# Optimization experiments

Hardware: AMD Instinct MI355X
Metric: run time of the kernel (lower is better)

## Reference

```python
import jax, jax.numpy as jnp
import numpy as np
import math

N_RAYS = 16384
HIDDEN = 32
Z_BOUNDS = (0.1, 1.0, 10.0)
STEPS_FIRST = (128, 64)
N_IMPORTANCE = 128
ALPHA_IMP = 0.02
INNER, OUTER = 1.0, 2.0


def _uniform_z_log():
    # get_uniform_z_vals: per-segment log10 linspace, endpoint excluded like torch code
    segs = []
    for i in range(len(STEPS_FIRST)):
        lo, hi = math.log10(Z_BOUNDS[i]), math.log10(Z_BOUNDS[i + 1])
        segs.append(np.linspace(lo, hi - (hi - lo) / STEPS_FIRST[i], STEPS_FIRST[i], dtype=np.float32))
    return jnp.asarray(np.concatenate(segs))


def _density(x, Wd1, bd1, Wd2, bd2):
    hfeat = jax.nn.relu(x @ Wd1 + bd1)            # [N,S,HIDDEN]
    sigma = jax.nn.softplus(hfeat @ Wd2 + bd2)[..., 0]  # [N,S]
    return sigma, hfeat


def _mip_scale(x):
    # mipnerf360_scale with translation_center = 0
    dist = jnp.linalg.norm(x, axis=-1, keepdims=True)
    scale = jnp.where(dist > INNER, (OUTER - (OUTER - INNER) / dist) / dist, 1.0)
    return x * scale


def _sample_points(rays_o, rays_d, z_vals):
    pts = rays_o[:, None, :] + rays_d[:, None, :] * z_vals[..., None]  # [N,S,3]
    dirs = rays_d / jnp.linalg.norm(rays_d, axis=-1, keepdims=True)
    return pts, jnp.broadcast_to(dirs[:, None, :], pts.shape)


def _weights_from_sigma(sigmas, z_log):
    # render_rays_log compositing: delta[:, -1] = 0
    delta = jnp.concatenate([z_log[:, 1:] - z_log[:, :-1], jnp.zeros_like(z_log[:, :1])], axis=-1)
    alpha = 1.0 - jnp.exp(-sigmas * delta)
    alpha_shift = jnp.concatenate([jnp.zeros_like(alpha[:, :1]), alpha[:, :-1]], axis=-1)
    weights = alpha * jnp.cumprod(1.0 - alpha_shift, axis=-1)
    return weights


def _reweight(weights):
    z = jnp.zeros_like(weights[:, :1])
    wp = jnp.concatenate([z, weights, z], axis=-1)
    w = 0.5 * (jnp.maximum(wp[:, :-2], wp[:, 1:-1]) + jnp.maximum(wp[:, 1:-1], wp[:, 2:]))
    w = w + ALPHA_IMP / w.shape[-1]
    total = sum(STEPS_FIRST)
    seg_scale = jnp.concatenate([jnp.full((s,), s / total, w.dtype) for s in STEPS_FIRST])
    w = w * seg_scale
    return w / jnp.sum(w, axis=-1, keepdims=True)


def _sample_pdf(z_vals, weights, key):
    n_rays = z_vals.shape[0]
    cdf = jnp.cumsum(weights, axis=-1)
    z_mid = 0.5 * (z_vals[:, :-1] + z_vals[:, 1:])
    u = jnp.linspace(0.0, 1.0 - 1.0 / N_IMPORTANCE, N_IMPORTANCE, dtype=z_vals.dtype)
    u = u[None, :] + jax.random.uniform(key, (n_rays, N_IMPORTANCE), dtype=z_vals.dtype) / N_IMPORTANCE
    u = u * (cdf[:, -2:-1] - cdf[:, 1:2]) + cdf[:, 1:2]
    inds = jax.vmap(lambda c, uu: jnp.searchsorted(c, uu, side='right'))(cdf[:, 1:-2], u) + 1
    g = lambda arr, idx: jnp.take_along_axis(arr, idx, axis=1)
    cdf_b, cdf_a = g(cdf, inds - 1), g(cdf, inds)
    t = (u - cdf_b) / (cdf_a - cdf_b)
    zb, za = g(z_mid, inds - 1), g(z_mid, inds)
    return zb + (za - zb) * t


def _forward(n, h, w, K, E, bg_color, Wd1, bd1, Wd2, bd2, Wc1, bc1, Wc2, bc2):
    # get_rays
    dirs = jnp.stack([w + 0.5, h + 0.5, jnp.ones_like(w)], axis=-1)        # [N,3]
    cam_dirs = dirs @ jnp.linalg.inv(K).T
    rays_d = jnp.einsum('nij,nj->ni', E[:, :3, :3], cam_dirs)
    rays_o = E[:, :3, -1]
    # efficient_sampling (no-grad coarse pass)
    n_rays = rays_o.shape[0]
    z_log_c = jnp.broadcast_to(_uniform_z_log()[None, :], (n_rays, sum(STEPS_FIRST)))
    z_c = jnp.power(10.0, z_log_c)
    xyz_c, _ = _sample_points(rays_o, rays_d, z_c)
    sig_c, _ = _density(_mip_scale(xyz_c), Wd1, bd1, Wd2, bd2)
    w_c = _weights_from_sigma(sig_c, z_log_c)
    w_re = _reweight(w_c)
    z_log_f = jax.lax.stop_gradient(_sample_pdf(z_log_c, w_re, jax.random.key(42)))
    z_f = jnp.power(10.0, z_log_f)
    # fine pass through model
    xyz, dirs_f = _sample_points(rays_o, rays_d, z_f)
    sigma, hfeat = _density(_mip_scale(xyz), Wd1, bd1, Wd2, bd2)
    feat = jnp.concatenate([hfeat, dirs_f], axis=-1)
    rgbs = jax.nn.sigmoid(jax.nn.relu(feat @ Wc1 + bc1) @ Wc2 + bc2)       # [N,S,3]
    weights = _weights_from_sigma(sigma, z_log_f)
    image = jnp.sum(weights[..., None] * rgbs, axis=-2)
    invdepth = jnp.sum(weights / z_f, axis=-1)
    image = image + (1.0 - jnp.sum(weights, axis=-1, keepdims=True)) * bg_color
    lo, hi = math.log10(Z_BOUNDS[0]), math.log10(Z_BOUNDS[-1])
    z_log_s = (z_log_f - lo) / (hi - lo)
    return image, weights, z_log_s, invdepth


def setup_inputs() -> dict:
    key = jax.random.key(0)
    ks = jax.random.split(key, 12)
    N = N_RAYS
    h = jax.random.uniform(ks[0], (N,), dtype=jnp.float32) * 1080.0
    w = jax.random.uniform(ks[1], (N,), dtype=jnp.float32) * 1920.0
    f = 1000.0
    K = jnp.array([[f, 0.0, 960.0], [0.0, f, 540.0], [0.0, 0.0, 1.0]], jnp.float32)
    t = jax.random.normal(ks[2], (N, 3), dtype=jnp.float32) * 0.1
    E = jnp.tile(jnp.eye(4, dtype=jnp.float32)[None], (N, 1, 1)).at[:, :3, 3].set(t)
    n = jax.random.randint(ks[3], (N,), 0, 100)
    bg_color = jax.random.uniform(ks[4], (3,), dtype=jnp.float32)
    Wd1 = jax.random.normal(ks[5], (3, HIDDEN), dtype=jnp.float32) * 0.5
    bd1 = jnp.zeros((HIDDEN,), jnp.float32)
    Wd2 = jax.random.normal(ks[6], (HIDDEN, 1), dtype=jnp.float32) * 0.3
    bd2 = jnp.zeros((1,), jnp.float32)
    Wc1 = jax.random.normal(ks[7], (HIDDEN + 3, HIDDEN), dtype=jnp.float32) * 0.3
    bc1 = jnp.zeros((HIDDEN,), jnp.float32)
    Wc2 = jax.random.normal(ks[8], (HIDDEN, 3), dtype=jnp.float32) * 0.3
    bc2 = jnp.zeros((3,), jnp.float32)
    return {"n": n, "h": h, "w": w, "K": K, "E": E, "bg_color": bg_color,
            "Wd1": Wd1, "bd1": bd1, "Wd2": Wd2, "bd2": bd2,
            "Wc1": Wc1, "bc1": bc1, "Wc2": Wc2, "bc2": bc2}


def reference(n, h, w, K, E, bg_color, Wd1, bd1, Wd2, bd2, Wc1, bc1, Wc2, bc2):
    return _forward(n, h, w, K, E, bg_color, Wd1, bd1, Wd2, bd2, Wc1, bc1, Wc2, bc2)
```

## Files before the change

kernel.cpp:

```cpp
#include <hip/hip_runtime.h>
#include <stdint.h>

#define SC 192
#define SF 128
#define NT 128

#define WD1   0
#define BD1   96
#define WD2   128
#define BD2   160
#define BC2   161
#define NV4   164
#define W24   292
#define KIV   420
#define WDF   432
#define SWTOT 448

#define WS_FRAG_OFF 2048
#define WS_NEED     4096

#define RGBS 4

using half8 = __attribute__((ext_vector_type(8))) _Float16;
using f32x4 = __attribute__((ext_vector_type(4))) float;
using f32x2 = __attribute__((ext_vector_type(2))) float;

__device__ __forceinline__ float zlog_c(int t) {
  return (t < 128) ? (-1.0f + (float)t * 0.0078125f)
                   : ((float)(t - 128) * 0.015625f);
}
__device__ __forceinline__ float delta_c(int t) {
  if (t >= SC - 1) return 0.0f;
  return zlog_c(t + 1) - zlog_c(t);
}

__device__ __forceinline__ float fast_rcp(float x) { return __builtin_amdgcn_rcpf(x); }
__device__ __forceinline__ float fast_rsq(float x) { return __builtin_amdgcn_rsqf(x); }
__device__ __forceinline__ float exp10_f(float x) { return __expf(x * 2.30258509299f); }
__device__ __forceinline__ float softplus_f(float x) {
  return fmaxf(x, 0.0f) + __logf(1.0f + __expf(-fabsf(x)));
}

__device__ __forceinline__ f32x2 pk_fma2(f32x2 a, f32x2 b, f32x2 c) {
  f32x2 d;
  asm("v_pk_fma_f32 %0, %1, %2, %3" : "=v"(d) : "v"(a), "v"(b), "v"(c));
  return d;
}
__device__ __forceinline__ f32x2 pk_add2(f32x2 a, f32x2 b) {
  f32x2 d;
  asm("v_pk_add_f32 %0, %1, %2" : "=v"(d) : "v"(a), "v"(b));
  return d;
}

__device__ __forceinline__ uint32_t pk2h(float a, float b) {
  auto p = __builtin_amdgcn_cvt_pkrtz(a, b);
  uint32_t u; __builtin_memcpy(&u, &p, 4); return u;
}
__device__ __forceinline__ unsigned short f2h(float f) {
  _Float16 h = (_Float16)f;
  unsigned short us; __builtin_memcpy(&us, &h, 2); return us;
}

__device__ __forceinline__ float4 ldsf4(const float* p) { return *(const float4*)p; }

__device__ __forceinline__ float wave_scan_mul(float v, int lane) {
#pragma unroll
  for (int d = 1; d < 64; d <<= 1) {
    float o = __shfl_up(v, d, 64);
    if (lane >= d) v *= o;
  }
  return v;
}
__device__ __forceinline__ float wave_scan_add(float v, int lane) {
#pragma unroll
  for (int d = 1; d < 64; d <<= 1) {
    float o = __shfl_up(v, d, 64);
    if (lane >= d) v += o;
  }
  return v;
}

template <int CTRL, int RM>
__device__ __forceinline__ float dpp_upd(float old, float v) {
  return __int_as_float(__builtin_amdgcn_update_dpp(
      __float_as_int(old), __float_as_int(v), CTRL, RM, 0xf, false));
}
__device__ __forceinline__ float dpp_scan_mul(float v) {
  v *= dpp_upd<0x111, 0xf>(1.0f, v);
  v *= dpp_upd<0x112, 0xf>(1.0f, v);
  v *= dpp_upd<0x114, 0xf>(1.0f, v);
  v *= dpp_upd<0x118, 0xf>(1.0f, v);
  v *= dpp_upd<0x142, 0xa>(1.0f, v);
  v *= dpp_upd<0x143, 0xc>(1.0f, v);
  return v;
}
__device__ __forceinline__ float dpp_scan_add(float v) {
  v += dpp_upd<0x111, 0xf>(0.0f, v);
  v += dpp_upd<0x112, 0xf>(0.0f, v);
  v += dpp_upd<0x114, 0xf>(0.0f, v);
  v += dpp_upd<0x118, 0xf>(0.0f, v);
  v += dpp_upd<0x142, 0xa>(0.0f, v);
  v += dpp_upd<0x143, 0xc>(0.0f, v);
  return v;
}
template <int CTRL, int RM>
__device__ __forceinline__ f32x2 dpp_upd2(f32x2 v) {
  f32x2 r;
  r.x = dpp_upd<CTRL, RM>(0.0f, v.x);
  r.y = dpp_upd<CTRL, RM>(0.0f, v.y);
  return r;
}
__device__ __forceinline__ f32x2 dpp_scan_add2(f32x2 v) {
  v = pk_add2(v, dpp_upd2<0x111, 0xf>(v));
  v = pk_add2(v, dpp_upd2<0x112, 0xf>(v));
  v = pk_add2(v, dpp_upd2<0x114, 0xf>(v));
  v = pk_add2(v, dpp_upd2<0x118, 0xf>(v));
  v = pk_add2(v, dpp_upd2<0x142, 0xa>(v));
  v = pk_add2(v, dpp_upd2<0x143, 0xc>(v));
  return v;
}

__device__ __forceinline__ int hperm(int i, int ntf) {
  return 8 * (i >> 2) + (i & 3) + ntf * 4;
}

__device__ __forceinline__ void threefry2x32_k42(uint32_t& x0, uint32_t& x1) {
  const uint32_t ks0 = 0u, ks1 = 42u;
  const uint32_t ks2 = ks0 ^ ks1 ^ 0x1BD11BDAu;
  const uint32_t ks[3] = {ks0, ks1, ks2};
  const int rot[2][4] = {{13, 15, 26, 6}, {17, 29, 16, 24}};
  x0 += ks[0];
  x1 += ks[1];
#pragma unroll
  for (int i = 0; i < 5; ++i) {
#pragma unroll
    for (int j = 0; j < 4; ++j) {
      x0 += x1;
      const int r = rot[i & 1][j];
      x1 = (x1 << r) | (x1 >> (32 - r));
      x1 ^= x0;
    }
    x0 += ks[(i + 1) % 3];
    x1 += ks[(i + 2) % 3] + (uint32_t)(i + 1);
  }
}

__global__ __launch_bounds__(NT) void pack_weights(
    const float* __restrict__ K,
    const float* __restrict__ Wd1, const float* __restrict__ bd1,
    const float* __restrict__ Wd2, const float* __restrict__ bd2,
    const float* __restrict__ Wc1, const float* __restrict__ bc1,
    const float* __restrict__ Wc2, const float* __restrict__ bc2,
    float* __restrict__ wsf) {
  const int t = threadIdx.x;
  for (int i = t; i < 96; i += NT) wsf[WD1 + i] = Wd1[i];
  for (int i = t; i < 32; i += NT) { wsf[BD1 + i] = bd1[i]; wsf[WD2 + i] = Wd2[i]; }
  if (t == 0) {
    wsf[BD2] = bd2[0];
    wsf[BC2 + 0] = bc2[0]; wsf[BC2 + 1] = bc2[1]; wsf[BC2 + 2] = bc2[2];
    const float k00 = K[0], k01 = K[1], k02 = K[2];
    const float k10 = K[3], k11 = K[4], k12 = K[5];
    const float k20 = K[6], k21 = K[7], k22 = K[8];
    const float det = k00 * (k11 * k22 - k12 * k21)
                    - k01 * (k10 * k22 - k12 * k20)
                    + k02 * (k10 * k21 - k11 * k20);
    const float id = 1.0f / det;
    wsf[KIV + 0] =  (k11 * k22 - k12 * k21) * id;
    wsf[KIV + 1] = -(k01 * k22 - k02 * k21) * id;
    wsf[KIV + 2] =  (k01 * k12 - k02 * k11) * id;
    wsf[KIV + 3] = -(k10 * k22 - k12 * k20) * id;
    wsf[KIV + 4] =  (k00 * k22 - k02 * k20) * id;
    wsf[KIV + 5] = -(k00 * k12 - k02 * k10) * id;
    wsf[KIV + 6] =  (k10 * k21 - k11 * k20) * id;
    wsf[KIV + 7] = -(k00 * k21 - k01 * k20) * id;
    wsf[KIV + 8] =  (k00 * k11 - k01 * k10) * id;
  }
  if (t < 32) {
    wsf[NV4 + t * 4 + 0] = bc1[t];
    wsf[NV4 + t * 4 + 1] = Wc1[32 * 32 + t];
    wsf[NV4 + t * 4 + 2] = Wc1[33 * 32 + t];
    wsf[NV4 + t * 4 + 3] = Wc1[34 * 32 + t];
  }
  if (t < 12) {
    const int m = t % 3, q = t / 3;
    uint32_t hw[4];
#pragma unroll
    for (int j2 = 0; j2 < 4; ++j2) {
      const int k0 = q * 8 + j2 * 2;
      hw[j2] = (uint32_t)f2h(Wc2[k0 * 3 + m])
             | ((uint32_t)f2h(Wc2[(k0 + 1) * 3 + m]) << 16);
    }
    ((uint4*)(wsf + W24))[t] = make_uint4(hw[0], hw[1], hw[2], hw[3]);
  }
  if (t < 4) {
    uint32_t hw[4];
#pragma unroll
    for (int j2 = 0; j2 < 4; ++j2) {
      const int k0 = t * 8 + j2 * 2;
      hw[j2] = pk2h(Wd2[k0], Wd2[k0 + 1]);
    }
    ((uint4*)(wsf + WDF))[t] = make_uint4(hw[0], hw[1], hw[2], hw[3]);
  }
  if (t < 64) {
    const int q_s = t >> 4;
    const int i = t & 15;
    uint4* frag = (uint4*)((char*)wsf + WS_FRAG_OFF);
#pragma unroll
    for (int nt = 0; nt < 2; ++nt) {
      const int n_s = hperm(i, nt);
      uint32_t hw[4];
#pragma unroll
      for (int j2 = 0; j2 < 4; ++j2) {
        const int k = q_s * 8 + j2 * 2;
        hw[j2] = (uint32_t)f2h(Wc1[k * 32 + n_s])
               | ((uint32_t)f2h(Wc1[(k + 1) * 32 + n_s]) << 16);
      }
      frag[t * 2 + nt] = make_uint4(hw[0], hw[1], hw[2], hw[3]);
    }
  }
}

template <bool USE_WS>
__global__ __launch_bounds__(NT, 8) void nerf_fwd(
    const float* __restrict__ hh, const float* __restrict__ ww,
    const float* __restrict__ K, const float* __restrict__ E,
    const float* __restrict__ bg,
    const float* __restrict__ Wd1, const float* __restrict__ bd1,
    const float* __restrict__ Wd2, const float* __restrict__ bd2,
    const float* __restrict__ Wc1, const float* __restrict__ bc1,
    const float* __restrict__ Wc2, const float* __restrict__ bc2,
    const float* __restrict__ wsf,
    float* __restrict__ out, int n_rays) {
  const int ray = blockIdx.x;
  const int t = threadIdx.x;
  const int lane = t & 63;
  const int wv = t >> 6;
  const int quad = lane >> 4;
  const int m15 = lane & 15;

  __shared__ __align__(16) float sw[SWTOT];
  __shared__ __align__(16) float s_A[32];
  __shared__ __align__(16) float s_B[32];
  __shared__ __align__(16) unsigned char u_buf[3072];
  float*    const s_w   = (float*)u_buf;
  float*    const s_cdf = (float*)(u_buf + 768);
  uint32_t* const s_mm  = (uint32_t*)u_buf;
  float*    const s_sig = (float*)(u_buf + 512);
  float*    const s_rgb = (float*)(u_buf + 1024);
  __shared__ float s_zlf[SF];
  __shared__ float s_tot[8];
  __shared__ float s_red[16];
  float* const s_dv = sw;

  if constexpr (USE_WS) {
    const float4* wsrc = (const float4*)wsf;
    float4* sdst = (float4*)sw;
    for (int i = t; i < SWTOT / 4; i += NT) sdst[i] = wsrc[i];
  } else {
    for (int i = t; i < 96; i += NT) sw[WD1 + i] = Wd1[i];
    for (int i = t; i < 32; i += NT) { sw[BD1 + i] = bd1[i]; sw[WD2 + i] = Wd2[i]; }
    if (t == 0) {
      sw[BD2] = bd2[0];
      sw[BC2 + 0] = bc2[0]; sw[BC2 + 1] = bc2[1]; sw[BC2 + 2] = bc2[2];
    }
    if (t < 32) {
      sw[NV4 + t * 4 + 0] = bc1[t];
      sw[NV4 + t * 4 + 1] = Wc1[32 * 32 + t];
      sw[NV4 + t * 4 + 2] = Wc1[33 * 32 + t];
      sw[NV4 + t * 4 + 3] = Wc1[34 * 32 + t];
    }
    if (t < 12) {
      const int m = t % 3, q = t / 3;
      uint32_t hw[4];
#pragma unroll
      for (int j2 = 0; j2 < 4; ++j2) {
        const int k0 = q * 8 + j2 * 2;
        hw[j2] = (uint32_t)f2h(Wc2[k0 * 3 + m])
               | ((uint32_t)f2h(Wc2[(k0 + 1) * 3 + m]) << 16);
      }
      ((uint4*)(sw + W24))[t] = make_uint4(hw[0], hw[1], hw[2], hw[3]);
    }
    if (t < 4) {
      uint32_t hw[4];
#pragma unroll
      for (int j2 = 0; j2 < 4; ++j2) {
        const int k0 = t * 8 + j2 * 2;
        hw[j2] = pk2h(Wd2[k0], Wd2[k0 + 1]);
      }
      ((uint4*)(sw + WDF))[t] = make_uint4(hw[0], hw[1], hw[2], hw[3]);
    }
  }

  float i00, i01, i02, i10, i11, i12, i20, i21, i22;
  if constexpr (USE_WS) {
    i00 = wsf[KIV + 0]; i01 = wsf[KIV + 1]; i02 = wsf[KIV + 2];
    i10 = wsf[KIV + 3]; i11 = wsf[KIV + 4]; i12 = wsf[KIV + 5];
    i20 = wsf[KIV + 6]; i21 = wsf[KIV + 7]; i22 = wsf[KIV + 8];
  } else {
    const float k00 = K[0], k01 = K[1], k02 = K[2];
    const float k10 = K[3], k11 = K[4], k12 = K[5];
    const float k20 = K[6], k21 = K[7], k22 = K[8];
    const float det = k00 * (k11 * k22 - k12 * k21)
                    - k01 * (k10 * k22 - k12 * k20)
                    + k02 * (k10 * k21 - k11 * k20);
    const float id = 1.0f / det;
    i00 =  (k11 * k22 - k12 * k21) * id;
    i01 = -(k01 * k22 - k02 * k21) * id;
    i02 =  (k01 * k12 - k02 * k11) * id;
    i10 = -(k10 * k22 - k12 * k20) * id;
    i11 =  (k00 * k22 - k02 * k20) * id;
    i12 = -(k00 * k12 - k02 * k10) * id;
    i20 =  (k10 * k21 - k11 * k20) * id;
    i21 = -(k00 * k21 - k01 * k20) * id;
    i22 =  (k00 * k11 - k01 * k10) * id;
  }

  const float dwx = ww[ray] + 0.5f;
  const float dwy = hh[ray] + 0.5f;
  const float cx = i00 * dwx + i01 * dwy + i02;
  const float cy = i10 * dwx + i11 * dwy + i12;
  const float cz = i20 * dwx + i21 * dwy + i22;
  const float* Er = E + (size_t)ray * 16;
  const float ox = Er[3], oy = Er[7], oz = Er[11];
  const float dx = Er[0] * cx + Er[1] * cy + Er[2] * cz;
  const float dy = Er[4] * cx + Er[5] * cy + Er[6] * cz;
  const float dz = Er[8] * cx + Er[9] * cy + Er[10] * cz;
  const float dd = dx * dx + dy * dy + dz * dz;
  const float inv_nrm = fast_rsq(dd);
  const float ndx = dx * inv_nrm, ndy = dy * inv_nrm, ndz = dz * inv_nrm;
  const float oo  = ox * ox + oy * oy + oz * oz;
  const float od2 = 2.0f * (ox * dx + oy * dy + oz * dz);

  if (t < 32) {
    const float w0 = Wd1[t], w1 = Wd1[32 + t], w2 = Wd1[64 + t];
    s_A[t] = ox * w0 + oy * w1 + oz * w2;
    s_B[t] = dx * w0 + dy * w1 + dz * w2;
  }

  __syncthreads();

  if (t < 32) {
    const float4 nv = ldsf4(sw + NV4 + t * 4);
    s_dv[t] = nv.x + ndx * nv.y + ndy * nv.z + ndz * nv.w;
  }

  const float bd2v = sw[BD2];
  float a0, v0, a1e = 0.0f, v1e = 1.0f;
  {
    float ms0, msz0, ms1 = 0.f, msz1 = 0.f;
    {
      const float z = exp10_f(zlog_c(t));
      const float d2 = fmaf(z, fmaf(z, dd, od2), oo);
      const float r = fast_rsq(fmaxf(d2, 1.0f));
      ms0 = (2.0f - r) * r;
      msz0 = ms0 * z;
    }
    if (wv == 0) {
      const float z = exp10_f((float)t * 0.015625f);
      const float d2 = fmaf(z, fmaf(z, dd, od2), oo);
      const float r = fast_rsq(fmaxf(d2, 1.0f));
      ms1 = (2.0f - r) * r;
      msz1 = ms1 * z;
    }
    const f32x2 msp0 = {ms0, ms0}, mszp0 = {msz0, msz0};
    const f32x2 msp1 = {ms1, ms1}, mszp1 = {msz1, msz1};
    f32x2 ac0a = {0.f, 0.f}, ac0b = {0.f, 0.f};
    f32x2 ac1a = {0.f, 0.f}, ac1b = {0.f, 0.f};
    if (wv == 0) {
#pragma unroll 2
      for (int c = 0; c < 8; ++c) {
        const int k4 = c * 4;
        const float4 A  = ldsf4(s_A + k4);
        const float4 B  = ldsf4(s_B + k4);
        const float4 b  = ldsf4(sw + BD1 + k4);
        const float4 wd = ldsf4(sw + WD2 + k4);
        const f32x2 Axy = {A.x, A.y}, Azw = {A.z, A.w};
        const f32x2 Bxy = {B.x, B.y}, Bzw = {B.z, B.w};
        const f32x2 bxy = {b.x, b.y}, bzw = {b.z, b.w};
        const f32x2 wxy = {wd.x, wd.y}, wzw = {wd.z, wd.w};
        f32x2 p;
        p = pk_fma2(mszp0, Bxy, pk_fma2(msp0, Axy, bxy));
        p.x = fmaxf(p.x, 0.f); p.y = fmaxf(p.y, 0.f);
        ac0a = pk_fma2(p, wxy, ac0a);
        p = pk_fma2(mszp0, Bzw, pk_fma2(msp0, Azw, bzw));
        p.x = fmaxf(p.x, 0.f); p.y = fmaxf(p.y, 0.f);
        ac0b = pk_fma2(p, wzw, ac0b);
        p = pk_fma2(mszp1, Bxy, pk_fma2(msp1, Axy, bxy));
        p.x = fmaxf(p.x, 0.f); p.y = fmaxf(p.y, 0.f);
        ac1a = pk_fma2(p, wxy, ac1a);
        p = pk_fma2(mszp1, Bzw, pk_fma2(msp1, Azw, bzw));
        p.x = fmaxf(p.x, 0.f); p.y = fmaxf(p.y, 0.f);
        ac1b = pk_fma2(p, wzw, ac1b);
      }
    } else {
#pragma unroll 2
      for (int c = 0; c < 8; ++c) {
        const int k4 = c * 4;
        const float4 A  = ldsf4(s_A + k4);
        const float4 B  = ldsf4(s_B + k4);
        const float4 b  = ldsf4(sw + BD1 + k4);
        const float4 wd = ldsf4(sw + WD2 + k4);
        const f32x2 Axy = {A.x, A.y}, Azw = {A.z, A.w};
        const f32x2 Bxy = {B.x, B.y}, Bzw = {B.z, B.w};
        const f32x2 bxy = {b.x, b.y}, bzw = {b.z, b.w};
        const f32x2 wxy = {wd.x, wd.y}, wzw = {wd.z, wd.w};
        f32x2 p;
        p = pk_fma2(mszp0, Bxy, pk_fma2(msp0, Axy, bxy));
        p.x = fmaxf(p.x, 0.f); p.y = fmaxf(p.y, 0.f);
        ac0a = pk_fma2(p, wxy, ac0a);
        p = pk_fma2(mszp0, Bzw, pk_fma2(msp0, Azw, bzw));
        p.x = fmaxf(p.x, 0.f); p.y = fmaxf(p.y, 0.f);
        ac0b = pk_fma2(p, wzw, ac0b);
      }
    }
    const float acc0 = bd2v + ((ac0a.x + ac0a.y) + (ac0b.x + ac0b.y));
    v0 = __expf(-softplus_f(acc0) * delta_c(t));
    a0 = 1.0f - v0;
    if (wv == 0) {
      const float acc1 = bd2v + ((ac1a.x + ac1a.y) + (ac1b.x + ac1b.y));
      v1e = __expf(-softplus_f(acc1) * delta_c(128 + t));
      a1e = 1.0f - v1e;
    }
  }

  float i0 = wave_scan_mul(v0, lane);
  float i1 = 1.0f;
  if (wv == 0) i1 = wave_scan_mul(v1e, lane);
  if (lane == 63) s_tot[wv] = i0;
  if (wv == 0 && lane == 63) s_tot[2] = i1;
  __syncthreads();
  {
    const float preC1 = s_tot[0];
    const float preC2 = s_tot[0] * s_tot[1];
    float e0x = __shfl_up(i0, 1, 64); if (lane == 0) e0x = 1.0f;
    s_w[t] = a0 * e0x * (wv ? preC1 : 1.0f);
    if (wv == 0) {
      float e1x = __shfl_up(i1, 1, 64); if (lane == 0) e1x = 1.0f;
      s_w[128 + t] = a1e * e1x * preC2;
    }
  }
  __syncthreads();

  float wre0, wre1 = 0.0f;
  {
    const float wm = (t > 0) ? s_w[t - 1] : 0.0f;
    const float w0 = s_w[t];
    const float wp = s_w[t + 1];
    wre0 = 0.5f * (fmaxf(wm, w0) + fmaxf(w0, wp)) + (0.02f / 192.0f);
    wre0 *= (t < 128) ? (128.0f / 192.0f) : (64.0f / 192.0f);
  }
  if (wv == 0) {
    const int e = 128 + t;
    const float wm = s_w[e - 1];
    const float w0 = s_w[e];
    const float wp = (e < SC - 1) ? s_w[e + 1] : 0.0f;
    wre1 = 0.5f * (fmaxf(wm, w0) + fmaxf(w0, wp)) + (0.02f / 192.0f);
    wre1 *= (64.0f / 192.0f);
  }

  float s0 = wave_scan_add(wre0, lane);
  float s1 = 0.0f;
  if (wv == 0) s1 = wave_scan_add(wre1, lane);
  if (lane == 63) s_tot[4 + wv] = s0;
  if (wv == 0 && lane == 63) s_tot[6] = s1;
  __syncthreads();
  {
    const float T0 = s_tot[4], T1 = s_tot[5], T2 = s_tot[6];
    const float inv_total = fast_rcp(T0 + T1 + T2);
    s_cdf[t] = (s0 + (wv ? T0 : 0.0f)) * inv_total;
    if (wv == 0) s_cdf[128 + t] = (s1 + T0 + T1) * inv_total;
  }
  __syncthreads();

  float zlf, zf;
  {
    const uint32_t total = (uint32_t)n_rays * 128u;
    const uint32_t halfc = total >> 1;
    const uint32_t j = (uint32_t)ray * 128u + (uint32_t)t;
    uint32_t x0, x1;
    const bool first = (j < halfc);
    if (first) { x0 = j; x1 = j + halfc; } else { x0 = j - halfc; x1 = j; }
    threefry2x32_k42(x0, x1);
    const uint32_t bits = first ? x0 : x1;
    const float fr = __uint_as_float((bits >> 9) | 0x3f800000u) - 1.0f;

    float u = (float)t * 0.0078125f + fr * 0.0078125f;
    u = u * (s_cdf[190] - s_cdf[1]) + s_cdf[1];

    int lo = 0, hi = 189;
    while (lo < hi) {
      const int mid = (lo + hi) >> 1;
      if (s_cdf[1 + mid] <= u) lo = mid + 1; else hi = mid;
    }
    const int inds = lo + 1;
    const float cb = s_cdf[inds - 1], ca = s_cdf[inds];
    const float tt = (u - cb) * fast_rcp(ca - cb);
    const float zb = 0.5f * (zlog_c(inds - 1) + zlog_c(inds));
    const float za = 0.5f * (zlog_c(inds) + zlog_c(inds + 1));
    zlf = zb + (za - zb) * tt;
    s_zlf[t] = zlf;
    zf = exp10_f(zlf);
  }
  __syncthreads();

  {
    const float d2 = fmaf(zf, fmaf(zf, dd, od2), oo);
    const float r = fast_rsq(fmaxf(d2, 1.0f));
    const float msf = (2.0f - r) * r;
    s_mm[t] = pk2h(msf, msf * zf);
  }

  uint4 BhS0, BhS1, BhS2, BhS3;
  {
    const bool q0 = (quad == 0);
    const int ma = hperm(m15, 0), mb = hperm(m15, 1);
    uint4 fa = make_uint4(q0 ? pk2h(s_A[ma], s_B[ma]) : 0u, 0u, 0u, 0u);
    uint4 fb = make_uint4(q0 ? pk2h(s_A[mb], s_B[mb]) : 0u, 0u, 0u, 0u);
    const uint4 fdq = ((const uint4*)(sw + WDF))[quad];
    const bool r0 = (m15 == 0);
    uint4 fd;
    fd.x = r0 ? fdq.x : 0u; fd.y = r0 ? fdq.y : 0u;
    fd.z = r0 ? fdq.z : 0u; fd.w = r0 ? fdq.w : 0u;
    half8 Waug0, Waug1, WdF;
    __builtin_memcpy(&Waug0, &fa, 16);
    __builtin_memcpy(&Waug1, &fb, 16);
    __builtin_memcpy(&WdF, &fd, 16);
    const float4 bb0 = ldsf4(sw + BD1 + quad * 8);
    const float4 bb1 = ldsf4(sw + BD1 + quad * 8 + 4);

#pragma unroll
    for (int g = 0; g < 4; ++g) {
      const uint32_t mm = s_mm[wv * 64 + g * 16 + m15];
      uint4 bm = make_uint4((quad == 0) ? mm : 0u, 0u, 0u, 0u);
      half8 Bms; __builtin_memcpy(&Bms, &bm, 16);

      f32x4 ad0 = {bb0.x, bb0.y, bb0.z, bb0.w};
      f32x4 ad1 = {bb1.x, bb1.y, bb1.z, bb1.w};
      ad0 = __builtin_amdgcn_mfma_f32_16x16x32_f16(Waug0, Bms, ad0, 0, 0, 0);
      ad1 = __builtin_amdgcn_mfma_f32_16x16x32_f16(Waug1, Bms, ad1, 0, 0, 0);

      uint4 bh;
      bh.x = pk2h(fmaxf(ad0[0], 0.0f), fmaxf(ad0[1], 0.0f));
      bh.y = pk2h(fmaxf(ad0[2], 0.0f), fmaxf(ad0[3], 0.0f));
      bh.z = pk2h(fmaxf(ad1[0], 0.0f), fmaxf(ad1[1], 0.0f));
      bh.w = pk2h(fmaxf(ad1[2], 0.0f), fmaxf(ad1[3], 0.0f));
      if (g == 0) BhS0 = bh; else if (g == 1) BhS1 = bh;
      else if (g == 2) BhS2 = bh; else BhS3 = bh;

      half8 Bh; __builtin_memcpy(&Bh, &bh, 16);
      f32x4 as = {bd2v, bd2v, bd2v, bd2v};
      as = __builtin_amdgcn_mfma_f32_16x16x32_f16(WdF, Bh, as, 0, 0, 0);
      if (quad == 0) s_sig[wv * 64 + g * 16 + m15] = as[0];
    }
  }
  const float sigf = softplus_f(s_sig[t]);

  {
    half8 Whi0, Whi1;
    if constexpr (USE_WS) {
      const uint4* frag = (const uint4*)((const char*)wsf + WS_FRAG_OFF);
      uint4 q0v = frag[lane * 2 + 0];
      uint4 q1v = frag[lane * 2 + 1];
      __builtin_memcpy(&Whi0, &q0v, 16);
      __builtin_memcpy(&Whi1, &q1v, 16);
    } else {
#pragma unroll
      for (int nt = 0; nt < 2; ++nt) {
        const int n_s = hperm(m15, nt);
        uint32_t hw[4];
#pragma unroll
        for (int j2 = 0; j2 < 4; ++j2) {
          const int k = quad * 8 + j2 * 2;
          hw[j2] = (uint32_t)f2h(Wc1[k * 32 + n_s])
                 | ((uint32_t)f2h(Wc1[(k + 1) * 32 + n_s]) << 16);
        }
        uint4 q = make_uint4(hw[0], hw[1], hw[2], hw[3]);
        if (nt == 0) __builtin_memcpy(&Whi0, &q, 16);
        else         __builtin_memcpy(&Whi1, &q, 16);
      }
    }
    const float4 dv0 = ldsf4(s_dv + quad * 8);
    const float4 dv1 = ldsf4(s_dv + quad * 8 + 4);
    uint4 qf = ((const uint4*)(sw + W24))[quad * 3 + (m15 < 3 ? m15 : 0)];
    if (m15 >= 3) qf = make_uint4(0u, 0u, 0u, 0u);
    half8 W2f; __builtin_memcpy(&W2f, &qf, 16);
    const float bc2x = sw[BC2 + 0], bc2y = sw[BC2 + 1], bc2z = sw[BC2 + 2];

#pragma unroll
    for (int g = 0; g < 4; ++g) {
      uint4 bh = (g == 0) ? BhS0 : (g == 1) ? BhS1 : (g == 2) ? BhS2 : BhS3;
      half8 Bh; __builtin_memcpy(&Bh, &bh, 16);

      f32x4 c0 = {dv0.x, dv0.y, dv0.z, dv0.w};
      f32x4 c1 = {dv1.x, dv1.y, dv1.z, dv1.w};
      c0 = __builtin_amdgcn_mfma_f32_16x16x32_f16(Whi0, Bh, c0, 0, 0, 0);
      c1 = __builtin_amdgcn_mfma_f32_16x16x32_f16(Whi1, Bh, c1, 0, 0, 0);

      uint4 bw;
      bw.x = pk2h(fmaxf(c0[0], 0.0f), fmaxf(c0[1], 0.0f));
      bw.y = pk2h(fmaxf(c0[2], 0.0f), fmaxf(c0[3], 0.0f));
      bw.z = pk2h(fmaxf(c1[0], 0.0f), fmaxf(c1[1], 0.0f));
      bw.w = pk2h(fmaxf(c1[2], 0.0f), fmaxf(c1[3], 0.0f));
      half8 Bav; __builtin_memcpy(&Bav, &bw, 16);

      f32x4 c2 = {bc2x, bc2y, bc2z, 0.0f};
      c2 = __builtin_amdgcn_mfma_f32_16x16x32_f16(W2f, Bav, c2, 0, 0, 0);
      if (quad == 0) {
        const int scol = wv * 64 + g * 16 + m15;
        *(f32x4*)(s_rgb + scol * RGBS) = c2;
      }
    }
  }

  const float deltaf = (t < SF - 1) ? (s_zlf[t + 1] - zlf) : 0.0f;
  const float vf = __expf(-sigf * deltaf);
  const float af = 1.0f - vf;
  float fi = dpp_scan_mul(vf);
  if (lane == 63) s_tot[wv] = fi;
  __syncthreads();
  float efx = __shfl_up(fi, 1, 64); if (lane == 0) efx = 1.0f;
  const float wf = af * efx * (wv ? s_tot[0] : 1.0f);

  float* o_img = out;
  float* o_w   = out + (size_t)n_rays * 3;
  float* o_z   = out + (size_t)n_rays * (3 + 128);
  float* o_inv = out + (size_t)n_rays * (3 + 256);

  o_w[(size_t)ray * 128 + t] = wf;
  o_z[(size_t)ray * 128 + t] = (zlf + 1.0f) * 0.5f;

  const float4 rgbv = ldsf4(s_rgb + t * RGBS);
  const float sr = fast_rcp(1.0f + __expf(-rgbv.x));
  const float sg = fast_rcp(1.0f + __expf(-rgbv.y));
  const float sb = fast_rcp(1.0f + __expf(-rgbv.z));

  f32x2 p01 = {wf * sr, wf * sg};
  f32x2 p23 = {wf * sb, wf};
  float r4 = wf * fast_rcp(zf);
  p01 = dpp_scan_add2(p01);
  p23 = dpp_scan_add2(p23);
  r4 = dpp_scan_add(r4);
  if (lane == 63) {
    float* p = &s_red[wv * 5];
    p[0] = p01.x; p[1] = p01.y; p[2] = p23.x; p[3] = p23.y; p[4] = r4;
  }
  __syncthreads();
  if (t == 0) {
    const float accw = s_red[3] + s_red[8];
    const float bgw = 1.0f - accw;
    o_img[(size_t)ray * 3 + 0] = (s_red[0] + s_red[5]) + bgw * bg[0];
    o_img[(size_t)ray * 3 + 1] = (s_red[1] + s_red[6]) + bgw * bg[1];
    o_img[(size_t)ray * 3 + 2] = (s_red[2] + s_red[7]) + bgw * bg[2];
    o_inv[ray] = s_red[4] + s_red[9];
  }
}

extern "C" void kernel_launch(void* const* d_in, const int* in_sizes, int n_in,
                              void* d_out, int out_size, void* d_ws, size_t ws_size,
                              hipStream_t stream) {
  const float* h   = (const float*)d_in[1];
  const float* w   = (const float*)d_in[2];
  const float* K   = (const float*)d_in[3];
  const float* E   = (const float*)d_in[4];
  const float* bg  = (const float*)d_in[5];
  const float* Wd1 = (const float*)d_in[6];
  const float* bd1 = (const float*)d_in[7];
  const float* Wd2 = (const float*)d_in[8];
  const float* bd2 = (const float*)d_in[9];
  const float* Wc1 = (const float*)d_in[10];
  const float* bc1 = (const float*)d_in[11];
  const float* Wc2 = (const float*)d_in[12];
  const float* bc2 = (const float*)d_in[13];
  const int n_rays = in_sizes[1];
  float* wsf = (float*)d_ws;

  if (ws_size >= WS_NEED) {
    pack_weights<<<1, NT, 0, stream>>>(K, Wd1, bd1, Wd2, bd2, Wc1, bc1, Wc2, bc2, wsf);
    nerf_fwd<true><<<n_rays, NT, 0, stream>>>(h, w, K, E, bg, Wd1, bd1, Wd2, bd2,
                                              Wc1, bc1, Wc2, bc2, wsf,
                                              (float*)d_out, n_rays);
  } else {
    nerf_fwd<false><<<n_rays, NT, 0, stream>>>(h, w, K, E, bg, Wd1, bd1, Wd2, bd2,
                                               Wc1, bc1, Wc2, bc2, nullptr,
                                               (float*)d_out, n_rays);
  }
}
```

Before: 64.90 us.

## Use 192 threads per ray block to balance coarse-sample work across three waves

Raises the block from two to three 64-lane waves so each of the 192 coarse samples gets its own thread. Previously wave 0 did double work on samples 128-191. The coarse density, scans, reweighting and CDF are now uniform across waves, while the fine-sample stage is guarded to the first 128 threads. This removes the per-wave imbalance and divergent branches, but the third wave sits idle through the fine MLP stage and the larger block may reduce how many blocks fit per CU.

```diff
diff --git a/kernel.cpp b/kernel.cpp
--- a/kernel.cpp
+++ b/kernel.cpp
@@ -3,7 +3,7 @@
 
 #define SC 192
 #define SF 128
-#define NT 128
+#define NT 192
 
 #define WD1   0
 #define BD1   96
@@ -345,135 +345,75 @@
   }
 
   const float bd2v = sw[BD2];
-  float a0, v0, a1e = 0.0f, v1e = 1.0f;
+  float a0, v0;
   {
-    float ms0, msz0, ms1 = 0.f, msz1 = 0.f;
-    {
-      const float z = exp10_f(zlog_c(t));
-      const float d2 = fmaf(z, fmaf(z, dd, od2), oo);
-      const float r = fast_rsq(fmaxf(d2, 1.0f));
-      ms0 = (2.0f - r) * r;
-      msz0 = ms0 * z;
-    }
-    if (wv == 0) {
-      const float z = exp10_f((float)t * 0.015625f);
-      const float d2 = fmaf(z, fmaf(z, dd, od2), oo);
-      const float r = fast_rsq(fmaxf(d2, 1.0f));
-      ms1 = (2.0f - r) * r;
-      msz1 = ms1 * z;
-    }
+    const float z = exp10_f(zlog_c(t));
+    const float d2 = fmaf(z, fmaf(z, dd, od2), oo);
+    const float r = fast_rsq(fmaxf(d2, 1.0f));
+    const float ms0 = (2.0f - r) * r;
+    const float msz0 = ms0 * z;
     const f32x2 msp0 = {ms0, ms0}, mszp0 = {msz0, msz0};
-    const f32x2 msp1 = {ms1, ms1}, mszp1 = {msz1, msz1};
     f32x2 ac0a = {0.f, 0.f}, ac0b = {0.f, 0.f};
-    f32x2 ac1a = {0.f, 0.f}, ac1b = {0.f, 0.f};
-    if (wv == 0) {
 #pragma unroll 2
-      for (int c = 0; c < 8; ++c) {
-        const int k4 = c * 4;
-        const float4 A  = ldsf4(s_A + k4);
-        const float4 B  = ldsf4(s_B + k4);
-        const float4 b  = ldsf4(sw + BD1 + k4);
-        const float4 wd = ldsf4(sw + WD2 + k4);
-        const f32x2 Axy = {A.x, A.y}, Azw = {A.z, A.w};
-        const f32x2 Bxy = {B.x, B.y}, Bzw = {B.z, B.w};
-        const f32x2 bxy = {b.x, b.y}, bzw = {b.z, b.w};
-        const f32x2 wxy = {wd.x, wd.y}, wzw = {wd.z, wd.w};
-        f32x2 p;
-        p = pk_fma2(mszp0, Bxy, pk_fma2(msp0, Axy, bxy));
-        p.x = fmaxf(p.x, 0.f); p.y = fmaxf(p.y, 0.f);
-        ac0a = pk_fma2(p, wxy, ac0a);
-        p = pk_fma2(mszp0, Bzw, pk_fma2(msp0, Azw, bzw));
-        p.x = fmaxf(p.x, 0.f); p.y = fmaxf(p.y, 0.f);
-        ac0b = pk_fma2(p, wzw, ac0b);
-        p = pk_fma2(mszp1, Bxy, pk_fma2(msp1, Axy, bxy));
-        p.x = fmaxf(p.x, 0.f); p.y = fmaxf(p.y, 0.f);
-        ac1a = pk_fma2(p, wxy, ac1a);
-        p = pk_fma2(mszp1, Bzw, pk_fma2(msp1, Azw, bzw));
-        p.x = fmaxf(p.x, 0.f); p.y = fmaxf(p.y, 0.f);
-        ac1b = pk_fma2(p, wzw, ac1b);
-      }
-    } else {
-#pragma unroll 2
-      for (int c = 0; c < 8; ++c) {
-        const int k4 = c * 4;
-        const float4 A  = ldsf4(s_A + k4);
-        const float4 B  = ldsf4(s_B + k4);
-        const float4 b  = ldsf4(sw + BD1 + k4);
-        const float4 wd = ldsf4(sw + WD2 + k4);
-        const f32x2 Axy = {A.x, A.y}, Azw = {A.z, A.w};
-        const f32x2 Bxy = {B.x, B.y}, Bzw = {B.z, B.w};
-        const f32x2 bxy = {b.x, b.y}, bzw = {b.z, b.w};
-        const f32x2 wxy = {wd.x, wd.y}, wzw = {wd.z, wd.w};
-        f32x2 p;
-        p = pk_fma2(mszp0, Bxy, pk_fma2(msp0, Axy, bxy));
-        p.x = fmaxf(p.x, 0.f); p.y = fmaxf(p.y, 0.f);
-        ac0a = pk_fma2(p, wxy, ac0a);
-        p = pk_fma2(mszp0, Bzw, pk_fma2(msp0, Azw, bzw));
-        p.x = fmaxf(p.x, 0.f); p.y = fmaxf(p.y, 0.f);
-        ac0b = pk_fma2(p, wzw, ac0b);
-      }
+    for (int c = 0; c < 8; ++c) {
+      const int k4 = c * 4;
+      const float4 A  = ldsf4(s_A + k4);
+      const float4 B  = ldsf4(s_B + k4);
+      const float4 b  = ldsf4(sw + BD1 + k4);
+      const float4 wd = ldsf4(sw + WD2 + k4);
+      const f32x2 Axy = {A.x, A.y}, Azw = {A.z, A.w};
+      const f32x2 Bxy = {B.x, B.y}, Bzw = {B.z, B.w};
+      const f32x2 bxy = {b.x, b.y}, bzw = {b.z, b.w};
+      const f32x2 wxy = {wd.x, wd.y}, wzw = {wd.z, wd.w};
+      f32x2 p;
+      p = pk_fma2(mszp0, Bxy, pk_fma2(msp0, Axy, bxy));
+      p.x = fmaxf(p.x, 0.f); p.y = fmaxf(p.y, 0.f);
+      ac0a = pk_fma2(p, wxy, ac0a);
+      p = pk_fma2(mszp0, Bzw, pk_fma2(msp0, Azw, bzw));
+      p.x = fmaxf(p.x, 0.f); p.y = fmaxf(p.y, 0.f);
+      ac0b = pk_fma2(p, wzw, ac0b);
     }
     const float acc0 = bd2v + ((ac0a.x + ac0a.y) + (ac0b.x + ac0b.y));
     v0 = __expf(-softplus_f(acc0) * delta_c(t));
     a0 = 1.0f - v0;
-    if (wv == 0) {
-      const float acc1 = bd2v + ((ac1a.x + ac1a.y) + (ac1b.x + ac1b.y));
-      v1e = __expf(-softplus_f(acc1) * delta_c(128 + t));
-      a1e = 1.0f - v1e;
-    }
   }
 
   float i0 = wave_scan_mul(v0, lane);
-  float i1 = 1.0f;
-  if (wv == 0) i1 = wave_scan_mul(v1e, lane);
   if (lane == 63) s_tot[wv] = i0;
-  if (wv == 0 && lane == 63) s_tot[2] = i1;
   __syncthreads();
   {
-    const float preC1 = s_tot[0];
-    const float preC2 = s_tot[0] * s_tot[1];
+    const float preC = (wv == 0) ? 1.0f
+                     : (wv == 1) ? s_tot[0]
+                                 : s_tot[0] * s_tot[1];
     float e0x = __shfl_up(i0, 1, 64); if (lane == 0) e0x = 1.0f;
-    s_w[t] = a0 * e0x * (wv ? preC1 : 1.0f);
-    if (wv == 0) {
-      float e1x = __shfl_up(i1, 1, 64); if (lane == 0) e1x = 1.0f;
-      s_w[128 + t] = a1e * e1x * preC2;
-    }
-  }
-  __syncthreads();
-
-  float wre0, wre1 = 0.0f;
+    s_w[t] = a0 * e0x * preC;
+  }
+  __syncthreads();
+
+  float wre0;
   {
     const float wm = (t > 0) ? s_w[t - 1] : 0.0f;
     const float w0 = s_w[t];
-    const float wp = s_w[t + 1];
+    const float wp = (t < SC - 1) ? s_w[t + 1] : 0.0f;
     wre0 = 0.5f * (fmaxf(wm, w0) + fmaxf(w0, wp)) + (0.02f / 192.0f);
     wre0 *= (t < 128) ? (128.0f / 192.0f) : (64.0f / 192.0f);
   }
-  if (wv == 0) {
-    const int e = 128 + t;
-    const float wm = s_w[e - 1];
-    const float w0 = s_w[e];
-    const float wp = (e < SC - 1) ? s_w[e + 1] : 0.0f;
-    wre1 = 0.5f * (fmaxf(wm, w0) + fmaxf(w0, wp)) + (0.02f / 192.0f);
-    wre1 *= (64.0f / 192.0f);
-  }
 
   float s0 = wave_scan_add(wre0, lane);
-  float s1 = 0.0f;
-  if (wv == 0) s1 = wave_scan_add(wre1, lane);
   if (lane == 63) s_tot[4 + wv] = s0;
-  if (wv == 0 && lane == 63) s_tot[6] = s1;
   __syncthreads();
   {
     const float T0 = s_tot[4], T1 = s_tot[5], T2 = s_tot[6];
     const float inv_total = fast_rcp(T0 + T1 + T2);
-    s_cdf[t] = (s0 + (wv ? T0 : 0.0f)) * inv_total;
-    if (wv == 0) s_cdf[128 + t] = (s1 + T0 + T1) * inv_total;
-  }
-  __syncthreads();
-
-  float zlf, zf;
-  {
+    const float c = (wv == 0) ? s0
+                  : (wv == 1) ? (s0 + T0)
+                              : (s0 + T0 + T1);
+    s_cdf[t] = c * inv_total;
+  }
+  __syncthreads();
+
+  float zlf = 0.0f, zf = 1.0f;
+  if (t < SF) {
     const uint32_t total = (uint32_t)n_rays * 128u;
     const uint32_t halfc = total >> 1;
     const uint32_t j = (uint32_t)ray * 128u + (uint32_t)t;
@@ -503,149 +443,154 @@
   }
   __syncthreads();
 
-  {
-    const float d2 = fmaf(zf, fmaf(zf, dd, od2), oo);
-    const float r = fast_rsq(fmaxf(d2, 1.0f));
-    const float msf = (2.0f - r) * r;
-    s_mm[t] = pk2h(msf, msf * zf);
-  }
-
-  uint4 BhS0, BhS1, BhS2, BhS3;
-  {
-    const bool q0 = (quad == 0);
-    const int ma = hperm(m15, 0), mb = hperm(m15, 1);
-    uint4 fa = make_uint4(q0 ? pk2h(s_A[ma], s_B[ma]) : 0u, 0u, 0u, 0u);
-    uint4 fb = make_uint4(q0 ? pk2h(s_A[mb], s_B[mb]) : 0u, 0u, 0u, 0u);
-    const uint4 fdq = ((const uint4*)(sw + WDF))[quad];
-    const bool r0 = (m15 == 0);
-    uint4 fd;
-    fd.x = r0 ? fdq.x : 0u; fd.y = r0 ? fdq.y : 0u;
-    fd.z = r0 ? fdq.z : 0u; fd.w = r0 ? fdq.w : 0u;
-    half8 Waug0, Waug1, WdF;
-    __builtin_memcpy(&Waug0, &fa, 16);
-    __builtin_memcpy(&Waug1, &fb, 16);
-    __builtin_memcpy(&WdF, &fd, 16);
-    const float4 bb0 = ldsf4(sw + BD1 + quad * 8);
-    const float4 bb1 = ldsf4(sw + BD1 + quad * 8 + 4);
-
-#pragma unroll
-    for (int g = 0; g < 4; ++g) {
-      const uint32_t mm = s_mm[wv * 64 + g * 16 + m15];
-      uint4 bm = make_uint4((quad == 0) ? mm : 0u, 0u, 0u, 0u);
-      half8 Bms; __builtin_memcpy(&Bms, &bm, 16);
-
-      f32x4 ad0 = {bb0.x, bb0.y, bb0.z, bb0.w};
-      f32x4 ad1 = {bb1.x, bb1.y, bb1.z, bb1.w};
-      ad0 = __builtin_amdgcn_mfma_f32_16x16x32_f16(Waug0, Bms, ad0, 0, 0, 0);
-      ad1 = __builtin_amdgcn_mfma_f32_16x16x32_f16(Waug1, Bms, ad1, 0, 0, 0);
-
-      uint4 bh;
-      bh.x = pk2h(fmaxf(ad0[0], 0.0f), fmaxf(ad0[1], 0.0f));
-      bh.y = pk2h(fmaxf(ad0[2], 0.0f), fmaxf(ad0[3], 0.0f));
-      bh.z = pk2h(fmaxf(ad1[0], 0.0f), fmaxf(ad1[1], 0.0f));
-      bh.w = pk2h(fmaxf(ad1[2], 0.0f), fmaxf(ad1[3], 0.0f));
-      if (g == 0) BhS0 = bh; else if (g == 1) BhS1 = bh;
-      else if (g == 2) BhS2 = bh; else BhS3 = bh;
-
-      half8 Bh; __builtin_memcpy(&Bh, &bh, 16);
-      f32x4 as = {bd2v, bd2v, bd2v, bd2v};
-      as = __builtin_amdgcn_mfma_f32_16x16x32_f16(WdF, Bh, as, 0, 0, 0);
-      if (quad == 0) s_sig[wv * 64 + g * 16 + m15] = as[0];
-    }
-  }
-  const float sigf = softplus_f(s_sig[t]);
-
-  {
-    half8 Whi0, Whi1;
-    if constexpr (USE_WS) {
-      const uint4* frag = (const uint4*)((const char*)wsf + WS_FRAG_OFF);
-      uint4 q0v = frag[lane * 2 + 0];
-      uint4 q1v = frag[lane * 2 + 1];
-      __builtin_memcpy(&Whi0, &q0v, 16);
-      __builtin_memcpy(&Whi1, &q1v, 16);
-    } else {
-#pragma unroll
-      for (int nt = 0; nt < 2; ++nt) {
-        const int n_s = hperm(m15, nt);
-        uint32_t hw[4];
-#pragma unroll
-        for (int j2 = 0; j2 < 4; ++j2) {
-          const int k = quad * 8 + j2 * 2;
-          hw[j2] = (uint32_t)f2h(Wc1[k * 32 + n_s])
-                 | ((uint32_t)f2h(Wc1[(k + 1) * 32 + n_s]) << 16);
+  float sigf = 0.0f, af = 0.0f, fi = 1.0f, vf = 1.0f;
+  if (t < SF) {
+    {
+      const float d2 = fmaf(zf, fmaf(zf, dd, od2), oo);
+      const float r = fast_rsq(fmaxf(d2, 1.0f));
+      const float msf = (2.0f - r) * r;
+      s_mm[t] = pk2h(msf, msf * zf);
+    }
+
+    uint4 BhS0, BhS1, BhS2, BhS3;
+    {
+      const bool q0 = (quad == 0);
+      const int ma = hperm(m15, 0), mb = hperm(m15, 1);
+      uint4 fa = make_uint4(q0 ? pk2h(s_A[ma], s_B[ma]) : 0u, 0u, 0u, 0u);
+      uint4 fb = make_uint4(q0 ? pk2h(s_A[mb], s_B[mb]) : 0u, 0u, 0u, 0u);
+      const uint4 fdq = ((const uint4*)(sw + WDF))[quad];
+      const bool r0 = (m15 == 0);
+      uint4 fd;
+      fd.x = r0 ? fdq.x : 0u; fd.y = r0 ? fdq.y : 0u;
+      fd.z = r0 ? fdq.z : 0u; fd.w = r0 ? fdq.w : 0u;
+      half8 Waug0, Waug1, WdF2;
+      __builtin_memcpy(&Waug0, &fa, 16);
+      __builtin_memcpy(&Waug1, &fb, 16);
+      __builtin_memcpy(&WdF2, &fd, 16);
+      const float4 bb0 = ldsf4(sw + BD1 + quad * 8);
+      const float4 bb1 = ldsf4(sw + BD1 + quad * 8 + 4);
+
+#pragma unroll
+      for (int g = 0; g < 4; ++g) {
+        const uint32_t mm = s_mm[wv * 64 + g * 16 + m15];
+        uint4 bm = make_uint4((quad == 0) ? mm : 0u, 0u, 0u, 0u);
+        half8 Bms; __builtin_memcpy(&Bms, &bm, 16);
+
+        f32x4 ad0 = {bb0.x, bb0.y, bb0.z, bb0.w};
+        f32x4 ad1 = {bb1.x, bb1.y, bb1.z, bb1.w};
+        ad0 = __builtin_amdgcn_mfma_f32_16x16x32_f16(Waug0, Bms, ad0, 0, 0, 0);
+        ad1 = __builtin_amdgcn_mfma_f32_16x16x32_f16(Waug1, Bms, ad1, 0, 0, 0);
+
+        uint4 bh;
+        bh.x = pk2h(fmaxf(ad0[0], 0.0f), fmaxf(ad0[1], 0.0f));
+        bh.y = pk2h(fmaxf(ad0[2], 0.0f), fmaxf(ad0[3], 0.0f));
+        bh.z = pk2h(fmaxf(ad1[0], 0.0f), fmaxf(ad1[1], 0.0f));
+        bh.w = pk2h(fmaxf(ad1[2], 0.0f), fmaxf(ad1[3], 0.0f));
+        if (g == 0) BhS0 = bh; else if (g == 1) BhS1 = bh;
+        else if (g == 2) BhS2 = bh; else BhS3 = bh;
+
+        half8 Bh; __builtin_memcpy(&Bh, &bh, 16);
+        f32x4 as = {bd2v, bd2v, bd2v, bd2v};
+        as = __builtin_amdgcn_mfma_f32_16x16x32_f16(WdF2, Bh, as, 0, 0, 0);
+        if (quad == 0) s_sig[wv * 64 + g * 16 + m15] = as[0];
+      }
+    }
+    sigf = softplus_f(s_sig[t]);
+
+    {
+      half8 Whi0, Whi1;
+      if constexpr (USE_WS) {
+        const uint4* frag = (const uint4*)((const char*)wsf + WS_FRAG_OFF);
+        uint4 q0v = frag[lane * 2 + 0];
+        uint4 q1v = frag[lane * 2 + 1];
+        __builtin_memcpy(&Whi0, &q0v, 16);
+        __builtin_memcpy(&Whi1, &q1v, 16);
+      } else {
+#pragma unroll
+        for (int nt = 0; nt < 2; ++nt) {
+          const int n_s = hperm(m15, nt);
+          uint32_t hw[4];
+#pragma unroll
+          for (int j2 = 0; j2 < 4; ++j2) {
+            const int k = quad * 8 + j2 * 2;
+            hw[j2] = (uint32_t)f2h(Wc1[k * 32 + n_s])
+                   | ((uint32_t)f2h(Wc1[(k + 1) * 32 + n_s]) << 16);
+          }
+          uint4 q = make_uint4(hw[0], hw[1], hw[2], hw[3]);
+          if (nt == 0) __builtin_memcpy(&Whi0, &q, 16);
+          else         __builtin_memcpy(&Whi1, &q, 16);
         }
-        uint4 q = make_uint4(hw[0], hw[1], hw[2], hw[3]);
-        if (nt == 0) __builtin_memcpy(&Whi0, &q, 16);
-        else         __builtin_memcpy(&Whi1, &q, 16);
       }
-    }
-    const float4 dv0 = ldsf4(s_dv + quad * 8);
-    const float4 dv1 = ldsf4(s_dv + quad * 8 + 4);
-    uint4 qf = ((const uint4*)(sw + W24))[quad * 3 + (m15 < 3 ? m15 : 0)];
-    if (m15 >= 3) qf = make_uint4(0u, 0u, 0u, 0u);
-    half8 W2f; __builtin_memcpy(&W2f, &qf, 16);
-    const float bc2x = sw[BC2 + 0], bc2y = sw[BC2 + 1], bc2z = sw[BC2 + 2];
-
-#pragma unroll
-    for (int g = 0; g < 4; ++g) {
-      uint4 bh = (g == 0) ? BhS0 : (g == 1) ? BhS1 : (g == 2) ? BhS2 : BhS3;
-      half8 Bh; __builtin_memcpy(&Bh, &bh, 16);
-
-      f32x4 c0 = {dv0.x, dv0.y, dv0.z, dv0.w};
-      f32x4 c1 = {dv1.x, dv1.y, dv1.z, dv1.w};
-      c0 = __builtin_amdgcn_mfma_f32_16x16x32_f16(Whi0, Bh, c0, 0, 0, 0);
-      c1 = __builtin_amdgcn_mfma_f32_16x16x32_f16(Whi1, Bh, c1, 0, 0, 0);
-
-      uint4 bw;
-      bw.x = pk2h(fmaxf(c0[0], 0.0f), fmaxf(c0[1], 0.0f));
-      bw.y = pk2h(fmaxf(c0[2], 0.0f), fmaxf(c0[3], 0.0f));
-      bw.z = pk2h(fmaxf(c1[0], 0.0f), fmaxf(c1[1], 0.0f));
-      bw.w = pk2h(fmaxf(c1[2], 0.0f), fmaxf(c1[3], 0.0f));
-      half8 Bav; __builtin_memcpy(&Bav, &bw, 16);
-
-      f32x4 c2 = {bc2x, bc2y, bc2z, 0.0f};
-      c2 = __builtin_amdgcn_mfma_f32_16x16x32_f16(W2f, Bav, c2, 0, 0, 0);
-      if (quad == 0) {
-        const int scol = wv * 64 + g * 16 + m15;
-        *(f32x4*)(s_rgb + scol * RGBS) = c2;
+      const float4 dv0 = ldsf4(s_dv + quad * 8);
+      const float4 dv1 = ldsf4(s_dv + quad * 8 + 4);
+      uint4 qf = ((const uint4*)(sw + W24))[quad * 3 + (m15 < 3 ? m15 : 0)];
+      if (m15 >= 3) qf = make_uint4(0u, 0u, 0u, 0u);
+      half8 W2f; __builtin_memcpy(&W2f, &qf, 16);
+      const float bc2x = sw[BC2 + 0], bc2y = sw[BC2 + 1], bc2z = sw[BC2 + 2];
+
+#pragma unroll
+      for (int g = 0; g < 4; ++g) {
+        uint4 bh = (g == 0) ? BhS0 : (g == 1) ? BhS1 : (g == 2) ? BhS2 : BhS3;
+        half8 Bh; __builtin_memcpy(&Bh, &bh, 16);
+
+        f32x4 c0 = {dv0.x, dv0.y, dv0.z, dv0.w};
+        f32x4 c1 = {dv1.x, dv1.y, dv1.z, dv1.w};
+        c0 = __builtin_amdgcn_mfma_f32_16x16x32_f16(Whi0, Bh, c0, 0, 0, 0);
+        c1 = __builtin_amdgcn_mfma_f32_16x16x32_f16(Whi1, Bh, c1, 0, 0, 0);
+
+        uint4 bw;
+        bw.x = pk2h(fmaxf(c0[0], 0.0f), fmaxf(c0[1], 0.0f));
+        bw.y = pk2h(fmaxf(c0[2], 0.0f), fmaxf(c0[3], 0.0f));
+        bw.z = pk2h(fmaxf(c1[0], 0.0f), fmaxf(c1[1], 0.0f));
+        bw.w = pk2h(fmaxf(c1[2], 0.0f), fmaxf(c1[3], 0.0f));
+        half8 Bav; __builtin_memcpy(&Bav, &bw, 16);
+
+        f32x4 c2 = {bc2x, bc2y, bc2z, 0.0f};
+        c2 = __builtin_amdgcn_mfma_f32_16x16x32_f16(W2f, Bav, c2, 0, 0, 0);
+        if (quad == 0) {
+          const int scol = wv * 64 + g * 16 + m15;
+          *(f32x4*)(s_rgb + scol * RGBS) = c2;
+        }
       }
     }
-  }
-
-  const float deltaf = (t < SF - 1) ? (s_zlf[t + 1] - zlf) : 0.0f;
-  const float vf = __expf(-sigf * deltaf);
-  const float af = 1.0f - vf;
-  float fi = dpp_scan_mul(vf);
-  if (lane == 63) s_tot[wv] = fi;
-  __syncthreads();
-  float efx = __shfl_up(fi, 1, 64); if (lane == 0) efx = 1.0f;
-  const float wf = af * efx * (wv ? s_tot[0] : 1.0f);
-
-  float* o_img = out;
-  float* o_w   = out + (size_t)n_rays * 3;
-  float* o_z   = out + (size_t)n_rays * (3 + 128);
-  float* o_inv = out + (size_t)n_rays * (3 + 256);
-
-  o_w[(size_t)ray * 128 + t] = wf;
-  o_z[(size_t)ray * 128 + t] = (zlf + 1.0f) * 0.5f;
-
-  const float4 rgbv = ldsf4(s_rgb + t * RGBS);
-  const float sr = fast_rcp(1.0f + __expf(-rgbv.x));
-  const float sg = fast_rcp(1.0f + __expf(-rgbv.y));
-  const float sb = fast_rcp(1.0f + __expf(-rgbv.z));
-
-  f32x2 p01 = {wf * sr, wf * sg};
-  f32x2 p23 = {wf * sb, wf};
-  float r4 = wf * fast_rcp(zf);
-  p01 = dpp_scan_add2(p01);
-  p23 = dpp_scan_add2(p23);
-  r4 = dpp_scan_add(r4);
-  if (lane == 63) {
-    float* p = &s_red[wv * 5];
-    p[0] = p01.x; p[1] = p01.y; p[2] = p23.x; p[3] = p23.y; p[4] = r4;
+
+    const float deltaf = (t < SF - 1) ? (s_zlf[t + 1] - zlf) : 0.0f;
+    vf = __expf(-sigf * deltaf);
+    af = 1.0f - vf;
+    fi = dpp_scan_mul(vf);
+    if (lane == 63) s_tot[wv] = fi;
+  }
+  __syncthreads();
+
+  if (t < SF) {
+    float efx = __shfl_up(fi, 1, 64); if (lane == 0) efx = 1.0f;
+    const float wf = af * efx * (wv ? s_tot[0] : 1.0f);
+
+    float* o_w   = out + (size_t)n_rays * 3;
+    float* o_z   = out + (size_t)n_rays * (3 + 128);
+    o_w[(size_t)ray * 128 + t] = wf;
+    o_z[(size_t)ray * 128 + t] = (zlf + 1.0f) * 0.5f;
+
+    const float4 rgbv = ldsf4(s_rgb + t * RGBS);
+    const float sr = fast_rcp(1.0f + __expf(-rgbv.x));
+    const float sg = fast_rcp(1.0f + __expf(-rgbv.y));
+    const float sb = fast_rcp(1.0f + __expf(-rgbv.z));
+
+    f32x2 p01 = {wf * sr, wf * sg};
+    f32x2 p23 = {wf * sb, wf};
+    float r4 = wf * fast_rcp(zf);
+    p01 = dpp_scan_add2(p01);
+    p23 = dpp_scan_add2(p23);
+    r4 = dpp_scan_add(r4);
+    if (lane == 63) {
+      float* p = &s_red[wv * 5];
+      p[0] = p01.x; p[1] = p01.y; p[2] = p23.x; p[3] = p23.y; p[4] = r4;
+    }
   }
   __syncthreads();
   if (t == 0) {
+    float* o_img = out;
+    float* o_inv = out + (size_t)n_rays * (3 + 256);
     const float accw = s_red[3] + s_red[8];
     const float bgw = 1.0f - accw;
     o_img[(size_t)ray * 3 + 0] = (s_red[0] + s_red[5]) + bgw * bg[0];
```

Result: slower. 72.15 us (+11.2%).
